# Optimization experiments

Measured on AMD Instinct MI355X. Metric: run time of the kernel, lower is better.

Reference implementation:

```python
import jax, jax.numpy as jnp
import numpy as np

NUM_HEADS = 16
WINDOW = 256
DIM = 1024


def setup_inputs() -> dict:
    key = jax.random.key(0)
    k1, k2, k3, k4, k5 = jax.random.split(key, 5)
    B, L, D = 2, 2048, DIM
    s = 1.0 / np.sqrt(D)
    return {
        "x": jax.random.normal(k1, (B, L, D), dtype=jnp.float32),
        "in_proj_w": jax.random.uniform(k2, (3 * D, D), dtype=jnp.float32, minval=-s, maxval=s),
        "in_proj_b": jax.random.uniform(k3, (3 * D,), dtype=jnp.float32, minval=-s, maxval=s),
        "out_w": jax.random.uniform(k4, (D, D), dtype=jnp.float32, minval=-s, maxval=s),
        "out_b": jax.random.uniform(k5, (D,), dtype=jnp.float32, minval=-s, maxval=s),
    }


def reference(x, in_proj_w, in_proj_b, out_w, out_b):
    B, L, D = x.shape
    H = NUM_HEADS
    hd = D // H

    # combined qkv projection, as in nn.MultiheadAttention
    qkv = x @ in_proj_w.T + in_proj_b          # [B, L, 3D]
    q, k, v = jnp.split(qkv, 3, axis=-1)
    q = q.reshape(B, L, H, hd).transpose(0, 2, 1, 3)  # [B, H, L, hd]
    k = k.reshape(B, L, H, hd).transpose(0, 2, 1, 3)
    v = v.reshape(B, L, H, hd).transpose(0, 2, 1, 3)

    scale = 1.0 / jnp.sqrt(jnp.asarray(hd, dtype=x.dtype))
    scores = jnp.einsum("bhqd,bhkd->bhqk", q * scale, k)  # [B, H, L, L]

    # sliding-window causal mask: allowed iff i-window < j <= i
    i = jnp.arange(L)[:, None]
    j = jnp.arange(L)[None, :]
    allowed = (j <= i) & (j > i - WINDOW)                  # [L, L]
    scores = jnp.where(allowed[None, None], scores, -jnp.inf)

    attn = jax.nn.softmax(scores, axis=-1)
    out = jnp.einsum("bhqk,bhkd->bhqd", attn, v)           # [B, H, L, hd]
    out = out.transpose(0, 2, 1, 3).reshape(B, L, D)
    return out @ out_w.T + out_b
```

## Files before the change

kernel.cpp:

```cpp
#include <hip/hip_runtime.h>


#define SEQ_L 2048
#define WIN   256

typedef __bf16 bf16x8 __attribute__((ext_vector_type(8)));
typedef float  f32x4  __attribute__((ext_vector_type(4)));

template<int X> struct ic { static constexpr int v = X; };

__device__ __forceinline__ unsigned short f32_to_bf16(float f) {
  unsigned int u = __float_as_uint(f);
  u += 0x7FFFu + ((u >> 16) & 1u);
  return (unsigned short)(u >> 16);
}

__device__ __forceinline__ void async16(const unsigned short* g, unsigned short* l) {
  __builtin_amdgcn_global_load_lds(
      (const __attribute__((address_space(1))) unsigned int*)g,
      (__attribute__((address_space(3))) unsigned int*)l, 16, 0, 0);
}

__global__ void cast_all(const float* __restrict__ x,  unsigned short* __restrict__ xo,
                         const float* __restrict__ w1, unsigned short* __restrict__ w1o,
                         const float* __restrict__ w2, unsigned short* __restrict__ w2o) {
  int i = blockIdx.x * 256 + threadIdx.x;
  const float* in; unsigned short* out; int k;
  if (i < 1048576)       { in = x;  out = xo;  k = i; }
  else if (i < 1835008)  { in = w1; out = w1o; k = i - 1048576; }
  else                   { in = w2; out = w2o; k = i - 1835008; }
  float4 v = ((const float4*)in)[k];
  ushort4 o;
  o.x = f32_to_bf16(v.x); o.y = f32_to_bf16(v.y);
  o.z = f32_to_bf16(v.z); o.w = f32_to_bf16(v.w);
  ((ushort4*)out)[k] = o;
}

__global__ __launch_bounds__(512, 2) void gemm_qkv(
    const unsigned short* __restrict__ A,
    const unsigned short* __restrict__ Bt,
    const float* __restrict__ bias,
    unsigned short* __restrict__ C, int M, int N, int K)
{
  __shared__ unsigned short As[2][256 * 64];
  __shared__ unsigned short Bs[2][192 * 64];

  const int tid  = threadIdx.x;
  const int lane = tid & 63;
  const int w    = tid >> 6;
  const int wr   = w >> 2;
  const int wc   = w & 3;
  const int quad = lane >> 4;
  const int l16  = lane & 15;
  const int lrow = (lane >> 3) & 7;
  const int scol = (lane & 7) ^ lrow;

  const long m0 = (long)blockIdx.y * 256;
  const long n0 = (long)blockIdx.x * 192;

  f32x4 acc[8][3];
#pragma unroll
  for (int i = 0; i < 8; ++i)
#pragma unroll
    for (int j = 0; j < 3; ++j)
#pragma unroll
      for (int r = 0; r < 4; ++r) acc[i][j][r] = 0.0f;

  auto stA = [&](int buf, int c, int kc) {
    async16(A + (m0 + c * 64 + w * 8 + lrow) * (long)K + kc + scol * 8,
            &As[buf][(c * 64 + w * 8) * 64]);
  };
  auto stB = [&](int buf, int c, int kc) {
    async16(Bt + (n0 + c * 64 + w * 8 + lrow) * (long)K + kc + scol * 8,
            &Bs[buf][(c * 64 + w * 8) * 64]);
  };
  auto hA0 = [&](int buf, int kc) { stA(buf, 0, kc); stA(buf, 2, kc); };
  auto hA1 = [&](int buf, int kc) { stA(buf, 1, kc); stA(buf, 3, kc); };
  auto hB  = [&](int buf, int kc) { stB(buf, 0, kc); stB(buf, 1, kc); stB(buf, 2, kc); };

  auto rdA = [&](bf16x8 (&af)[4], int buf, int QM, int kh) {
#pragma unroll
    for (int mi = 0; mi < 4; ++mi) {
      int rr = wr * 128 + QM * 64 + mi * 16 + l16;
      af[mi] = *(const bf16x8*)&As[buf][rr * 64 + (((kh * 4 + quad) ^ (rr & 7)) << 3)];
    }
  };
  auto rdB = [&](bf16x8 (&bq)[3], int buf, int kh) {
#pragma unroll
    for (int ni = 0; ni < 3; ++ni) {
      int rb = wc * 48 + ni * 16 + l16;
      bq[ni] = *(const bf16x8*)&Bs[buf][rb * 64 + (((kh * 4 + quad) ^ (rb & 7)) << 3)];
    }
  };
  auto cluster = [&](bf16x8 (&af)[4], bf16x8 (&bq)[3], int mb) {
    __builtin_amdgcn_s_setprio(1);
#pragma unroll
    for (int mi = 0; mi < 4; ++mi)
#pragma unroll
      for (int ni = 0; ni < 3; ++ni)
        acc[mb + mi][ni] = __builtin_amdgcn_mfma_f32_16x16x32_bf16(
            bq[ni], af[mi], acc[mb + mi][ni], 0, 0, 0);
    __builtin_amdgcn_s_setprio(0);
  };
  auto lgkm0 = [] {
    asm volatile("s_waitcnt lgkmcnt(0)" ::: "memory");
    __builtin_amdgcn_sched_barrier(0);
  };
  auto vmw = [](auto n) {
    constexpr int V = decltype(n)::v;
    if constexpr (V == 7)      asm volatile("s_waitcnt vmcnt(7)" ::: "memory");
    else if constexpr (V == 2) asm volatile("s_waitcnt vmcnt(2)" ::: "memory");
    else if constexpr (V == 0) asm volatile("s_waitcnt vmcnt(0)" ::: "memory");
  };

  hA0(0, 0); hB(0, 0); hA1(0, 0); hA0(1, 64); hB(1, 64);
  asm volatile("s_waitcnt vmcnt(7)" ::: "memory");
  __builtin_amdgcn_s_barrier();

  auto tile = [&](int T, auto s1, auto s4, auto v1, auto v4) {
    const int buf = T & 1;
    bf16x8 af[4], bq0[3], bq1[3];
    rdA(af, buf, 0, 0);
    rdB(bq0, buf, 0);
    if constexpr (decltype(s1)::v) hA1(buf ^ 1, (T + 1) * 64);
    lgkm0();
    cluster(af, bq0, 0);
    vmw(v1);
    __builtin_amdgcn_s_barrier();
    rdA(af, buf, 1, 0);
    lgkm0();
    cluster(af, bq0, 4);
    rdA(af, buf, 0, 1);
    rdB(bq1, buf, 1);
    lgkm0();
    cluster(af, bq1, 0);
    __builtin_amdgcn_s_barrier();
    rdA(af, buf, 1, 1);
    if constexpr (decltype(s4)::v) { hA0(buf, (T + 2) * 64); hB(buf, (T + 2) * 64); }
    lgkm0();
    cluster(af, bq1, 4);
    vmw(v4);
    __builtin_amdgcn_s_barrier();
  };

  const int NT = K >> 6;
#pragma unroll 1
  for (int T = 0; T < NT - 2; ++T) tile(T, ic<1>{}, ic<1>{}, ic<7>{}, ic<7>{});
  tile(NT - 2, ic<1>{}, ic<0>{}, ic<7>{}, ic<2>{});
  tile(NT - 1, ic<0>{}, ic<0>{}, ic<0>{}, ic<-1>{});

#pragma unroll
  for (int ni = 0; ni < 3; ++ni) {
    const int nb = wc * 48 + ni * 16 + quad * 4;
    const float4 bv = *(const float4*)&bias[n0 + nb];
#pragma unroll
    for (int qm = 0; qm < 2; ++qm)
#pragma unroll
      for (int mi = 0; mi < 4; ++mi) {
        long m = m0 + wr * 128 + qm * 64 + mi * 16 + l16;
        f32x4 a = acc[qm * 4 + mi][ni];
        ushort4 o;
        o.x = f32_to_bf16(a[0] + bv.x);
        o.y = f32_to_bf16(a[1] + bv.y);
        o.z = f32_to_bf16(a[2] + bv.z);
        o.w = f32_to_bf16(a[3] + bv.w);
        *(ushort4*)&C[m * (long)N + n0 + nb] = o;
      }
  }
}

__global__ __launch_bounds__(512, 4) void gemm_opj(
    const unsigned short* __restrict__ A,
    const unsigned short* __restrict__ Bt,
    const float* __restrict__ bias,
    float* __restrict__ C, int M, int N, int K)
{
  __shared__ unsigned short As[2][128 * 64];
  __shared__ unsigned short Bs[2][128 * 64];

  const int tid  = threadIdx.x;
  const int lane = tid & 63;
  const int w    = tid >> 6;
  const int wr   = w >> 2;
  const int wc   = w & 3;
  const int quad = lane >> 4;
  const int l16  = lane & 15;
  const int lrow = (lane >> 3) & 7;
  const int scol = (lane & 7) ^ lrow;

  const long m0 = (long)blockIdx.y * 128;
  const long n0 = (long)blockIdx.x * 128;

  f32x4 acc[4][2];
#pragma unroll
  for (int i = 0; i < 4; ++i)
#pragma unroll
    for (int j = 0; j < 2; ++j)
#pragma unroll
      for (int r = 0; r < 4; ++r) acc[i][j][r] = 0.0f;

  auto stage = [&](int buf, int kc) {
#pragma unroll
    for (int c = 0; c < 2; ++c)
      async16(A + (m0 + c * 64 + w * 8 + lrow) * (long)K + kc + scol * 8,
              &As[buf][(c * 64 + w * 8) * 64]);
#pragma unroll
    for (int c = 0; c < 2; ++c)
      async16(Bt + (n0 + c * 64 + w * 8 + lrow) * (long)K + kc + scol * 8,
              &Bs[buf][(c * 64 + w * 8) * 64]);
  };

  auto rdA = [&](bf16x8 (&af)[4], int buf, int kh) {
#pragma unroll
    for (int mi = 0; mi < 4; ++mi) {
      int rr = wr * 64 + mi * 16 + l16;
      af[mi] = *(const bf16x8*)&As[buf][rr * 64 + (((kh * 4 + quad) ^ (rr & 7)) << 3)];
    }
  };
  auto rdB = [&](bf16x8 (&bq)[2], int buf, int kh) {
#pragma unroll
    for (int ni = 0; ni < 2; ++ni) {
      int rb = wc * 32 + ni * 16 + l16;
      bq[ni] = *(const bf16x8*)&Bs[buf][rb * 64 + (((kh * 4 + quad) ^ (rb & 7)) << 3)];
    }
  };
  auto cluster = [&](bf16x8 (&af)[4], bf16x8 (&bq)[2]) {
    __builtin_amdgcn_s_setprio(1);
#pragma unroll
    for (int mi = 0; mi < 4; ++mi)
#pragma unroll
      for (int ni = 0; ni < 2; ++ni)
        acc[mi][ni] = __builtin_amdgcn_mfma_f32_16x16x32_bf16(
            bq[ni], af[mi], acc[mi][ni], 0, 0, 0);
    __builtin_amdgcn_s_setprio(0);
  };
  auto lgkm0 = [] {
    asm volatile("s_waitcnt lgkmcnt(0)" ::: "memory");
    __builtin_amdgcn_sched_barrier(0);
  };

  stage(0, 0); stage(1, 64);
  asm volatile("s_waitcnt vmcnt(4)" ::: "memory");
  __builtin_amdgcn_s_barrier();

  auto tile = [&](int T, auto s, auto v) {
    const int buf = T & 1;
    bf16x8 af[4], bq[2];
    rdA(af, buf, 0);
    rdB(bq, buf, 0);
    lgkm0();
    cluster(af, bq);
    rdA(af, buf, 1);
    rdB(bq, buf, 1);
    lgkm0();
    __builtin_amdgcn_s_barrier();
    if constexpr (decltype(s)::v) stage(buf, (T + 2) * 64);
    cluster(af, bq);
    if constexpr (decltype(v)::v == 4)
      asm volatile("s_waitcnt vmcnt(4)" ::: "memory");
    else if constexpr (decltype(v)::v == 0)
      asm volatile("s_waitcnt vmcnt(0)" ::: "memory");
    __builtin_amdgcn_s_barrier();
  };

  const int NT = K >> 6;
#pragma unroll 1
  for (int T = 0; T < NT - 2; ++T) tile(T, ic<1>{}, ic<4>{});
  tile(NT - 2, ic<0>{}, ic<0>{});
  tile(NT - 1, ic<0>{}, ic<-1>{});

#pragma unroll
  for (int ni = 0; ni < 2; ++ni) {
    const int nb = wc * 32 + ni * 16 + quad * 4;
    const float4 bv = *(const float4*)&bias[n0 + nb];
#pragma unroll
    for (int mi = 0; mi < 4; ++mi) {
      long m = m0 + wr * 64 + mi * 16 + l16;
      f32x4 a = acc[mi][ni];
      float4 o;
      o.x = a[0] + bv.x;
      o.y = a[1] + bv.y;
      o.z = a[2] + bv.z;
      o.w = a[3] + bv.w;
      *(float4*)&C[m * (long)N + n0 + nb] = o;
    }
  }
}

__global__ __launch_bounds__(256) void attn_kernel(
    const unsigned short* __restrict__ qkv,
    unsigned short* __restrict__ aout)
{
  __shared__ unsigned short Ks[64 * 72];
  __shared__ unsigned short Vt[64 * 72];
  __shared__ unsigned short Ps[4 * 16 * 72];

  const int tid  = threadIdx.x;
  const int w    = tid >> 6;
  const int lane = tid & 63;
  const int quad = lane >> 4;
  const int l16  = lane & 15;

  const int blk = blockIdx.x;
  const int qb  = blk & 15;
  const int h   = (blk >> 4) & 15;
  const int b   = blk >> 8;

  const int  i0 = qb * 128;
  const long rowbase = (long)b * SEQ_L;

  bf16x8 aq[2][2];
#pragma unroll
  for (int sub = 0; sub < 2; ++sub) {
    const unsigned short* qp =
        qkv + (rowbase + i0 + sub * 64 + w * 16 + l16) * 3072 + h * 64 + quad * 8;
    aq[sub][0] = *(const bf16x8*)(qp);
    aq[sub][1] = *(const bf16x8*)(qp + 32);
  }

  f32x4 o[2][4];
  float l_i[2][4];
#pragma unroll
  for (int sub = 0; sub < 2; ++sub)
#pragma unroll
    for (int ni = 0; ni < 4; ++ni)
#pragma unroll
      for (int r = 0; r < 4; ++r) { o[sub][ni][r] = 0.0f; l_i[sub][r] = 0.0f; }

  unsigned short* psw = &Ps[w * 16 * 72];

  const int j_begin = (i0 >= WIN) ? i0 - WIN : 0;

  for (int j0 = j_begin; j0 < i0 + 128; j0 += 64) {
    __syncthreads();
#pragma unroll
    for (int p = 0; p < 2; ++p) {
      int c = p * 256 + tid, row = c >> 3, col8 = c & 7;
      const unsigned short* base = qkv + (rowbase + j0 + row) * 3072 + h * 64 + col8 * 8;
      *(uint4*)(&Ks[row * 72 + col8 * 8]) = *(const uint4*)(base + 1024);
      unsigned short tmp[8];
      *(uint4*)tmp = *(const uint4*)(base + 2048);
      int rsw = row ^ (col8 << 3);
#pragma unroll
      for (int e = 0; e < 8; ++e)
        Vt[(col8 * 8 + e) * 72 + rsw] = tmp[e];
    }
    __syncthreads();

    bf16x8 kf[4][2];
#pragma unroll
    for (int g = 0; g < 4; ++g) {
      kf[g][0] = *(const bf16x8*)(&Ks[(g * 16 + l16) * 72 + quad * 8]);
      kf[g][1] = *(const bf16x8*)(&Ks[(g * 16 + l16) * 72 + 32 + quad * 8]);
    }
    bf16x8 vf[2][4];
#pragma unroll
    for (int kk = 0; kk < 2; ++kk)
#pragma unroll
      for (int ni = 0; ni < 4; ++ni) {
        int d  = ni * 16 + l16;
        int rb = (kk * 32 + quad * 8) ^ (((d >> 3) & 7) << 3);
        vf[kk][ni] = *(const bf16x8*)(&Vt[d * 72 + rb]);
      }

#pragma unroll
    for (int sub = 0; sub < 2; ++sub) {
      const int i0s = i0 + sub * 64 + w * 16;
      if (j0 > i0s + 15) continue;
      if (j0 + 63 + WIN <= i0s) continue;

      f32x4 s[4];
#pragma unroll
      for (int g = 0; g < 4; ++g) {
        f32x4 z;
#pragma unroll
        for (int r = 0; r < 4; ++r) z[r] = 0.0f;
        z = __builtin_amdgcn_mfma_f32_16x16x32_bf16(aq[sub][0], kf[g][0], z, 0, 0, 0);
        z = __builtin_amdgcn_mfma_f32_16x16x32_bf16(aq[sub][1], kf[g][1], z, 0, 0, 0);
        s[g] = z;
      }
#pragma unroll
      for (int g = 0; g < 4; ++g) {
        int j = j0 + g * 16 + l16;
#pragma unroll
        for (int r = 0; r < 4; ++r) {
          int i = i0s + quad * 4 + r;
          bool ok = (j <= i) && (j > i - WIN);
          float e = ok ? __expf(s[g][r] * 0.125f) : 0.0f;
          psw[(quad * 4 + r) * 72 + g * 16 + l16] = f32_to_bf16(e);
          l_i[sub][r] += e;
        }
      }
      asm volatile("s_waitcnt lgkmcnt(0)" ::: "memory");
#pragma unroll
      for (int kk = 0; kk < 2; ++kk) {
        bf16x8 ap = *(const bf16x8*)(&psw[l16 * 72 + kk * 32 + quad * 8]);
#pragma unroll
        for (int ni = 0; ni < 4; ++ni)
          o[sub][ni] = __builtin_amdgcn_mfma_f32_16x16x32_bf16(ap, vf[kk][ni], o[sub][ni], 0, 0, 0);
      }
    }
  }

#pragma unroll
  for (int sub = 0; sub < 2; ++sub)
#pragma unroll
    for (int r = 0; r < 4; ++r) {
      float rs = l_i[sub][r];
      rs += __shfl_xor(rs, 1);
      rs += __shfl_xor(rs, 2);
      rs += __shfl_xor(rs, 4);
      rs += __shfl_xor(rs, 8);
      float inv_l = 1.0f / rs;
      long row = rowbase + i0 + sub * 64 + w * 16 + quad * 4 + r;
#pragma unroll
      for (int ni = 0; ni < 4; ++ni)
        aout[row * 1024 + h * 64 + ni * 16 + l16] = f32_to_bf16(o[sub][ni][r] * inv_l);
    }
}

extern "C" void kernel_launch(void* const* d_in, const int* in_sizes, int n_in,
                              void* d_out, int out_size, void* d_ws, size_t ws_size,
                              hipStream_t stream)
{
  const float* x  = (const float*)d_in[0];
  const float* w1 = (const float*)d_in[1];
  const float* b1 = (const float*)d_in[2];
  const float* w2 = (const float*)d_in[3];
  const float* b2 = (const float*)d_in[4];
  float* out = (float*)d_out;

  char* ws = (char*)d_ws;
  unsigned short* x_bf   = (unsigned short*)(ws);
  unsigned short* w1_bf  = (unsigned short*)(ws + 8388608);
  unsigned short* w2_bf  = (unsigned short*)(ws + 14680064);
  unsigned short* qkv_bf = (unsigned short*)(ws + 16777216);
  unsigned short* at_bf  = (unsigned short*)(ws + 41943040);

  cast_all<<<8192, 256, 0, stream>>>(x, x_bf, w1, w1_bf, w2, w2_bf);

  dim3 g1(3072 / 192, 4096 / 256);
  gemm_qkv<<<g1, 512, 0, stream>>>(x_bf, w1_bf, b1, qkv_bf, 4096, 3072, 1024);

  attn_kernel<<<512, 256, 0, stream>>>(qkv_bf, at_bf);

  dim3 g2(1024 / 128, 4096 / 128);
  gemm_opj<<<g2, 512, 0, stream>>>(at_bf, w2_bf, b2, out, 4096, 1024, 1024);
}
```

Measured before the change: 156.7 us.

## Double-buffer attention K/V tiles and hoist GEMM LDS fragment reads

The attention kernel now keeps two LDS buffers for K and V. The next tile is prefetched into registers during compute and written to the alternate buffer, which overlaps global loads with MFMA work and drops one barrier per iteration. The GEMM tile loop issues all A/B fragment reads early into separate registers and waits on partial lgkmcnt counts, so LDS latency can overlap MFMA clusters. This raises register pressure and LDS usage, which may reduce occupancy.

```diff
diff --git a/kernel.cpp b/kernel.cpp
--- a/kernel.cpp
+++ b/kernel.cpp
@@ -102,8 +102,11 @@
             bq[ni], af[mi], acc[mb + mi][ni], 0, 0, 0);
     __builtin_amdgcn_s_setprio(0);
   };
-  auto lgkm0 = [] {
-    asm volatile("s_waitcnt lgkmcnt(0)" ::: "memory");
+  auto lgkm = [](auto n) {
+    constexpr int V = decltype(n)::v;
+    if constexpr (V == 8)      asm volatile("s_waitcnt lgkmcnt(8)" ::: "memory");
+    else if constexpr (V == 4) asm volatile("s_waitcnt lgkmcnt(4)" ::: "memory");
+    else                       asm volatile("s_waitcnt lgkmcnt(0)" ::: "memory");
     __builtin_amdgcn_sched_barrier(0);
   };
   auto vmw = [](auto n) {
@@ -117,29 +120,28 @@
   asm volatile("s_waitcnt vmcnt(7)" ::: "memory");
   __builtin_amdgcn_s_barrier();
 
-  auto tile = [&](int T, auto s1, auto s4, auto v1, auto v4) {
+  auto tile = [&](int T, auto s1, auto s4, auto vS, auto vE) {
     const int buf = T & 1;
-    bf16x8 af[4], bq0[3], bq1[3];
-    rdA(af, buf, 0, 0);
-    rdB(bq0, buf, 0);
+    bf16x8 af00[4], af10[4], af01[4], af11[4], bq0[3], bq1[3];
+    rdA(af00, buf, 0, 0);
+    rdB(bq0,  buf, 0);
+    rdA(af01, buf, 0, 1);
+    rdB(bq1,  buf, 1);
     if constexpr (decltype(s1)::v) hA1(buf ^ 1, (T + 1) * 64);
-    lgkm0();
-    cluster(af, bq0, 0);
-    vmw(v1);
+    vmw(vS);
     __builtin_amdgcn_s_barrier();
-    rdA(af, buf, 1, 0);
-    lgkm0();
-    cluster(af, bq0, 4);
-    rdA(af, buf, 0, 1);
-    rdB(bq1, buf, 1);
-    lgkm0();
-    cluster(af, bq1, 0);
+    rdA(af10, buf, 1, 0);
+    rdA(af11, buf, 1, 1);
+    lgkm(ic<8>{});
+    cluster(af00, bq0, 0);
+    lgkm(ic<4>{});
+    cluster(af10, bq0, 4);
+    cluster(af01, bq1, 0);
+    lgkm(ic<0>{});
     __builtin_amdgcn_s_barrier();
-    rdA(af, buf, 1, 1);
     if constexpr (decltype(s4)::v) { hA0(buf, (T + 2) * 64); hB(buf, (T + 2) * 64); }
-    lgkm0();
-    cluster(af, bq1, 4);
-    vmw(v4);
+    cluster(af11, bq1, 4);
+    if constexpr (decltype(vE)::v >= 0) vmw(vE);
     __builtin_amdgcn_s_barrier();
   };
 
@@ -291,8 +293,8 @@
     const unsigned short* __restrict__ qkv,
     unsigned short* __restrict__ aout)
 {
-  __shared__ unsigned short Ks[64 * 72];
-  __shared__ unsigned short Vt[64 * 72];
+  __shared__ unsigned short Ks[2][64 * 72];
+  __shared__ unsigned short Vt[2][64 * 72];
   __shared__ unsigned short Ps[4 * 16 * 72];
 
   const int tid  = threadIdx.x;
@@ -330,28 +332,44 @@
   unsigned short* psw = &Ps[w * 16 * 72];
 
   const int j_begin = (i0 >= WIN) ? i0 - WIN : 0;
-
-  for (int j0 = j_begin; j0 < i0 + 128; j0 += 64) {
-    __syncthreads();
+  const int j_end   = i0 + 128;
+
+  uint4 nk[2], nv[2];
+  auto load_tile = [&](int j0) {
 #pragma unroll
     for (int p = 0; p < 2; ++p) {
       int c = p * 256 + tid, row = c >> 3, col8 = c & 7;
       const unsigned short* base = qkv + (rowbase + j0 + row) * 3072 + h * 64 + col8 * 8;
-      *(uint4*)(&Ks[row * 72 + col8 * 8]) = *(const uint4*)(base + 1024);
+      nk[p] = *(const uint4*)(base + 1024);
+      nv[p] = *(const uint4*)(base + 2048);
+    }
+  };
+  auto write_tile = [&](int bi) {
+#pragma unroll
+    for (int p = 0; p < 2; ++p) {
+      int c = p * 256 + tid, row = c >> 3, col8 = c & 7;
+      *(uint4*)(&Ks[bi][row * 72 + col8 * 8]) = nk[p];
       unsigned short tmp[8];
-      *(uint4*)tmp = *(const uint4*)(base + 2048);
+      *(uint4*)tmp = nv[p];
       int rsw = row ^ (col8 << 3);
 #pragma unroll
       for (int e = 0; e < 8; ++e)
-        Vt[(col8 * 8 + e) * 72 + rsw] = tmp[e];
-    }
-    __syncthreads();
-
+        Vt[bi][(col8 * 8 + e) * 72 + rsw] = tmp[e];
+    }
+  };
+
+  load_tile(j_begin);
+  write_tile(0);
+  if (j_begin + 64 < j_end) load_tile(j_begin + 64);
+  __syncthreads();
+
+  int cur = 0;
+  for (int j0 = j_begin; j0 < j_end; j0 += 64) {
     bf16x8 kf[4][2];
 #pragma unroll
     for (int g = 0; g < 4; ++g) {
-      kf[g][0] = *(const bf16x8*)(&Ks[(g * 16 + l16) * 72 + quad * 8]);
-      kf[g][1] = *(const bf16x8*)(&Ks[(g * 16 + l16) * 72 + 32 + quad * 8]);
+      kf[g][0] = *(const bf16x8*)(&Ks[cur][(g * 16 + l16) * 72 + quad * 8]);
+      kf[g][1] = *(const bf16x8*)(&Ks[cur][(g * 16 + l16) * 72 + 32 + quad * 8]);
     }
     bf16x8 vf[2][4];
 #pragma unroll
@@ -360,7 +378,7 @@
       for (int ni = 0; ni < 4; ++ni) {
         int d  = ni * 16 + l16;
         int rb = (kk * 32 + quad * 8) ^ (((d >> 3) & 7) << 3);
-        vf[kk][ni] = *(const bf16x8*)(&Vt[d * 72 + rb]);
+        vf[kk][ni] = *(const bf16x8*)(&Vt[cur][d * 72 + rb]);
       }
 
 #pragma unroll
@@ -400,6 +418,13 @@
           o[sub][ni] = __builtin_amdgcn_mfma_f32_16x16x32_bf16(ap, vf[kk][ni], o[sub][ni], 0, 0, 0);
       }
     }
+
+    if (j0 + 64 < j_end) {
+      write_tile(cur ^ 1);
+      if (j0 + 128 < j_end) load_tile(j0 + 128);
+    }
+    __syncthreads();
+    cur ^= 1;
   }
 
 #pragma unroll
```

Result: slower. 171.7 us (+9.6%).
